# Performance work log

Hardware: AMD Instinct MI355X
Metric: run time of the kernel (lower is better)

The kernel has to match this reference:

```python
import jax, jax.numpy as jnp
import numpy as np

ALPHA_R = 0.1  # leak rate of rate variable r
ALPHA_S = 0.2  # leak rate of synaptic current I

B, T, IN, H, OUT = 32, 2048, 256, 1024, 128


def setup_inputs() -> dict:
    key = jax.random.key(0)
    k1, k2, k3, k4 = jax.random.split(key, 4)
    x = jax.random.normal(k1, (B, T, IN), dtype=jnp.float32)
    # Orthogonal-ish init approximated by scaled gaussians (spectral radius ~1)
    Win = jax.random.normal(k2, (H, IN), dtype=jnp.float32) / np.sqrt(IN)
    Wrec = jax.random.normal(k3, (H, H), dtype=jnp.float32) / np.sqrt(H)
    Wout = jax.random.uniform(k4, (OUT, H), dtype=jnp.float32)
    return {"x": x, "Win": Win, "Wrec": Wrec, "Wout": Wout}


def reference(x, Win, Wrec, Wout):
    # x: [B, T, IN]. State kept batch-major [B, H] (torch code uses [H, B]; same math transposed).
    b = x.shape[0]
    h = Wrec.shape[0]
    WinT, WrecT, WoutT = Win.T, Wrec.T, Wout.T

    def step(carry, xt):
        I, r = carry
        I = (1.0 - ALPHA_S) * I + ALPHA_S * (r @ WrecT + xt @ WinT)
        # r_t = (1-a_r) r + a_r tanh(I_t)
        r = (1.0 - ALPHA_R) * r + ALPHA_R * jnp.tanh(I)
        return (I, r), r @ WoutT  # out_t: [B, OUT]

    init = (jnp.zeros((b, h), x.dtype), jnp.zeros((b, h), x.dtype))
    _, ys = jax.lax.scan(step, init, jnp.swapaxes(x, 0, 1))  # ys: [T, B, OUT]
    return jnp.swapaxes(ys, 0, 1)  # [B, T, OUT]
```

## Files before the change

kernel.cpp:

```cpp
#include <hip/hip_runtime.h>
#include <math.h>


#define T_STEPS 2048
#define B_SZ 32
#define IN_SZ 256
#define H_SZ 1024
#define OUT_SZ 128
#define WGS 256
#define NWG 256
#define PB_WORDS (B_SZ * (H_SZ / 2))
#define WS_WORDS (2 * PB_WORDS)

typedef unsigned int u32;
typedef u32 u32x4 __attribute__((ext_vector_type(4)));
typedef float f32x4 __attribute__((ext_vector_type(4)));
typedef short s16x8 __attribute__((ext_vector_type(8)));

__global__ void nrnn_init_ws(u32* __restrict__ ws) {
  const int i = blockIdx.x * blockDim.x + threadIdx.x;
  if (i < WS_WORDS) ws[i] = 0x00000001u;
}

__device__ __forceinline__ u32 bf16r(float x) {
  const u32 b = __float_as_uint(x);
  return (b + 0x7FFFu + ((b >> 16) & 1u)) >> 16;
}
__device__ __forceinline__ void st_sys_u32(u32* p, u32 v) {
  __hip_atomic_store(p, v, __ATOMIC_RELAXED, __HIP_MEMORY_SCOPE_SYSTEM);
}
__device__ __forceinline__ float tanh_fast(float x) {
  const float cx = fminf(fmaxf(x, -15.f), 15.f);
  const float e = __expf(2.f * cx);
  return (e - 1.f) * __builtin_amdgcn_rcpf(e + 1.f);
}

__global__ void __launch_bounds__(WGS, 1)
nrnn_main(const float* __restrict__ x, const float* __restrict__ Win,
          const float* __restrict__ Wrec, const float* __restrict__ Wout,
          float* __restrict__ out, float* __restrict__ ws) {
  const int tid = (int)threadIdx.x;
  const int hg  = tid >> 5;
  const int s   = tid & 31;
  const int wv  = tid >> 6;
  const int ln  = tid & 63;
  const int bg  = (int)blockIdx.x & 7;
  const int jb  = (int)blockIdx.x >> 3;

  u32* pbuf = (u32*)ws;
  const int b0 = bg * 4;

  __shared__ __align__(16) char r_lds[4 * 2048];
  __shared__ float wacc_lds[2][32][4];
  __shared__ float4 padlds[4800];

  if (__float_as_uint(x[0]) == 0x7F800001u) padlds[tid].x = 1.f;

  s16x8 wfrag[32];
  {
    const int g = (ln >> 4) & 3;
    const float* wp;
    if (wv < 2)       wp = Wrec + (size_t)(jb * 32 + wv * 16 + (ln & 15)) * H_SZ;
    else if (wv == 2) wp = Wout + (size_t)(jb * 4 + (ln & 3)) * H_SZ;
    else              wp = Wrec;
    #pragma unroll
    for (int st = 0; st < 32; ++st) {
      const int k0 = st * 32 + g * 8;
      const float4 c0 = *(const float4*)(wp + k0);
      const float4 c1 = *(const float4*)(wp + k0 + 4);
      s16x8 w;
      w[0] = (short)bf16r(c0.x); w[1] = (short)bf16r(c0.y);
      w[2] = (short)bf16r(c0.z); w[3] = (short)bf16r(c0.w);
      w[4] = (short)bf16r(c1.x); w[5] = (short)bf16r(c1.y);
      w[6] = (short)bf16r(c1.z); w[7] = (short)bf16r(c1.w);
      wfrag[st] = w;
    }
  }

  float4 wi4[4][2];
  #pragma unroll
  for (int hh = 0; hh < 4; ++hh) {
    const float* ip = Win + (size_t)(jb * 32 + hg * 4 + hh) * IN_SZ + s * 4;
    wi4[hh][0] = *(const float4*)(ip);
    wi4[hh][1] = *(const float4*)(ip + 128);
  }

  float Ist[4] = {0.f, 0.f, 0.f, 0.f};
  float rloc[4] = {0.f, 0.f, 0.f, 0.f};

  {
    float wacc[4][4];
    #pragma unroll
    for (int b = 0; b < 4; ++b)
      #pragma unroll
      for (int hh = 0; hh < 4; ++hh) wacc[b][hh] = 0.f;
    #pragma unroll
    for (int b = 0; b < 4; ++b) {
      const float* xp = x + ((size_t)(b0 + b) * T_STEPS) * IN_SZ + s * 4;
      const float4 x0 = *(const float4*)(xp);
      const float4 x1 = *(const float4*)(xp + 128);
      #pragma unroll
      for (int hh = 0; hh < 4; ++hh) {
        float4 w4 = wi4[hh][0];
        wacc[b][hh] = fmaf(w4.x, x0.x, wacc[b][hh]);
        wacc[b][hh] = fmaf(w4.y, x0.y, wacc[b][hh]);
        wacc[b][hh] = fmaf(w4.z, x0.z, wacc[b][hh]);
        wacc[b][hh] = fmaf(w4.w, x0.w, wacc[b][hh]);
        w4 = wi4[hh][1];
        wacc[b][hh] = fmaf(w4.x, x1.x, wacc[b][hh]);
        wacc[b][hh] = fmaf(w4.y, x1.y, wacc[b][hh]);
        wacc[b][hh] = fmaf(w4.z, x1.z, wacc[b][hh]);
        wacc[b][hh] = fmaf(w4.w, x1.w, wacc[b][hh]);
      }
    }
    #pragma unroll
    for (int m = 1; m <= 16; m <<= 1)
      #pragma unroll
      for (int b = 0; b < 4; ++b)
        #pragma unroll
        for (int hh = 0; hh < 4; ++hh)
          wacc[b][hh] += __shfl_xor(wacc[b][hh], m, 64);
    if (s < 16) wacc_lds[0][hg * 4 + (s & 3)][s >> 2] = wacc[s >> 2][s & 3];
  }

  auto poll_stage = [&](int tcur) {
    const u32 etag = (((u32)(tcur - 1)) >> 1) & 1u;
    const u32* gp = pbuf + (size_t)((tcur + 1) & 1) * PB_WORDS + (size_t)bg * 2048u;
    const u32* p0 = gp + 4 * tid;
    const u32* p1 = gp + 1024 + 4 * tid;
    u32x4 a0, a1;
    bool ok;
    do {
      asm volatile(
          "global_load_dwordx4 %0, %2, off sc0 sc1\n\t"
          "global_load_dwordx4 %1, %3, off sc0 sc1\n\t"
          "s_waitcnt vmcnt(0)"
          : "=&v"(a0), "=&v"(a1) : "v"(p0), "v"(p1) : "memory");
      u32 bad = 0;
      #pragma unroll
      for (int i = 0; i < 4; ++i) { bad |= a0[i] ^ etag; bad |= a1[i] ^ etag; }
      ok = ((bad & 1u) == 0u);
    } while (__any(!ok));
    const int bi0 = tid >> 7, bi1 = 2 + (tid >> 7);
    *(u32x4*)(r_lds + ((16 * tid) ^ ((bi0 & 3) << 4) ^ ((bi0 & 1) << 6))) = a0;
    *(u32x4*)(r_lds + ((4096 + 16 * tid) ^ ((bi1 & 3) << 4) ^ ((bi1 & 1) << 6))) = a1;
  };

  for (int t = 0; t < T_STEPS; ++t) {
    const int tt = (t + 1 < T_STEPS) ? (t + 1) : (T_STEPS - 1);
    float4 xv[4][2];
    #pragma unroll
    for (int b = 0; b < 4; ++b) {
      const float* xp = x + ((size_t)(b0 + b) * T_STEPS + (size_t)tt) * IN_SZ + s * 4;
      xv[b][0] = *(const float4*)(xp);
      xv[b][1] = *(const float4*)(xp + 128);
    }

    poll_stage(t);
    __syncthreads();

    f32x4 acc = {0.f, 0.f, 0.f, 0.f};
    if (wv <= 2) {
      const int beff = ln & 3;
      const int g16 = ((ln >> 4) & 3) * 16;
      const int bswz = ((beff & 3) << 4) | ((beff & 1) << 6);
      const char* rb = r_lds + beff * 2048;
      #pragma unroll
      for (int st = 0; st < 32; ++st) {
        const s16x8 bf = *(const s16x8*)(rb + ((st * 64 + g16) ^ bswz));
        acc = __builtin_amdgcn_mfma_f32_16x16x32_bf16(wfrag[st], bf, acc, 0, 0, 0);
      }
    }

    if (wv < 2 && (ln & 12) == 0) {
      const int b = ln & 3;
      const int g = ln >> 4;
      const int rbase = wv * 16 + g * 4;
      const u32 ptag = (((u32)t) >> 1) & 1u;
      u32 pk0, pk1;
      {
        float In0 = fmaf(0.2f, acc[0] + wacc_lds[t & 1][rbase + 0][b], 0.8f * Ist[0]);
        float In1 = fmaf(0.2f, acc[1] + wacc_lds[t & 1][rbase + 1][b], 0.8f * Ist[1]);
        float In2 = fmaf(0.2f, acc[2] + wacc_lds[t & 1][rbase + 2][b], 0.8f * Ist[2]);
        float In3 = fmaf(0.2f, acc[3] + wacc_lds[t & 1][rbase + 3][b], 0.8f * Ist[3]);
        Ist[0] = In0; Ist[1] = In1; Ist[2] = In2; Ist[3] = In3;
        rloc[0] = fmaf(0.1f, tanh_fast(In0), 0.9f * rloc[0]);
        rloc[1] = fmaf(0.1f, tanh_fast(In1), 0.9f * rloc[1]);
        rloc[2] = fmaf(0.1f, tanh_fast(In2), 0.9f * rloc[2]);
        rloc[3] = fmaf(0.1f, tanh_fast(In3), 0.9f * rloc[3]);
        pk0 = ((bf16r(rloc[1]) << 16) | (bf16r(rloc[0]) & 0xFFFFu));
        pk0 = (pk0 & ~1u) | ptag;
        pk1 = ((bf16r(rloc[3]) << 16) | (bf16r(rloc[2]) & 0xFFFFu));
        pk1 = (pk1 & ~1u) | ptag;
      }
      u32* pw = pbuf + (size_t)(t & 1) * PB_WORDS
                + (size_t)(b0 + b) * 512 + jb * 16 + wv * 8 + g * 2;
      st_sys_u32(pw, pk0);
      st_sys_u32(pw + 1, pk1);
    }

    if (wv == 2 && ln < 4 && t > 0) {
      #pragma unroll
      for (int reg = 0; reg < 4; ++reg)
        out[((size_t)(b0 + ln) * T_STEPS + (size_t)(t - 1)) * OUT_SZ + jb * 4 + reg] = acc[reg];
    }

    {
      float wacc[4][4];
      #pragma unroll
      for (int b = 0; b < 4; ++b)
        #pragma unroll
        for (int hh = 0; hh < 4; ++hh) wacc[b][hh] = 0.f;
      #pragma unroll
      for (int b = 0; b < 4; ++b) {
        const float4 x0 = xv[b][0];
        const float4 x1 = xv[b][1];
        #pragma unroll
        for (int hh = 0; hh < 4; ++hh) {
          float4 w4 = wi4[hh][0];
          wacc[b][hh] = fmaf(w4.x, x0.x, wacc[b][hh]);
          wacc[b][hh] = fmaf(w4.y, x0.y, wacc[b][hh]);
          wacc[b][hh] = fmaf(w4.z, x0.z, wacc[b][hh]);
          wacc[b][hh] = fmaf(w4.w, x0.w, wacc[b][hh]);
          w4 = wi4[hh][1];
          wacc[b][hh] = fmaf(w4.x, x1.x, wacc[b][hh]);
          wacc[b][hh] = fmaf(w4.y, x1.y, wacc[b][hh]);
          wacc[b][hh] = fmaf(w4.z, x1.z, wacc[b][hh]);
          wacc[b][hh] = fmaf(w4.w, x1.w, wacc[b][hh]);
        }
      }
      #pragma unroll
      for (int m = 1; m <= 16; m <<= 1)
        #pragma unroll
        for (int b = 0; b < 4; ++b)
          #pragma unroll
          for (int hh = 0; hh < 4; ++hh)
            wacc[b][hh] += __shfl_xor(wacc[b][hh], m, 64);
      if (s < 16)
        wacc_lds[(t + 1) & 1][hg * 4 + (s & 3)][s >> 2] = wacc[s >> 2][s & 3];
    }

    __syncthreads();
  }

  poll_stage(T_STEPS);
  __syncthreads();
  {
    f32x4 acc = {0.f, 0.f, 0.f, 0.f};
    if (wv == 2) {
      const int beff = ln & 3;
      const int g16 = ((ln >> 4) & 3) * 16;
      const int bswz = ((beff & 3) << 4) | ((beff & 1) << 6);
      const char* rb = r_lds + beff * 2048;
      #pragma unroll
      for (int st = 0; st < 32; ++st) {
        const s16x8 bf = *(const s16x8*)(rb + ((st * 64 + g16) ^ bswz));
        acc = __builtin_amdgcn_mfma_f32_16x16x32_bf16(wfrag[st], bf, acc, 0, 0, 0);
      }
      if (ln < 4) {
        #pragma unroll
        for (int reg = 0; reg < 4; ++reg)
          out[((size_t)(b0 + ln) * T_STEPS + (size_t)(T_STEPS - 1)) * OUT_SZ + jb * 4 + reg] = acc[reg];
      }
    }
  }
}

extern "C" void kernel_launch(void* const* d_in, const int* in_sizes, int n_in,
                              void* d_out, int out_size, void* d_ws, size_t ws_size,
                              hipStream_t stream) {
  const float* xp    = (const float*)d_in[0];
  const float* winp  = (const float*)d_in[1];
  const float* wrecp = (const float*)d_in[2];
  const float* woutp = (const float*)d_in[3];
  float* outp = (float*)d_out;
  float* wsp  = (float*)d_ws;

  nrnn_init_ws<<<(WS_WORDS + 255) / 256, 256, 0, stream>>>((u32*)d_ws);

  nrnn_main<<<dim3(NWG), dim3(WGS), 0, stream>>>(xp, winp, wrecp, woutp, outp, wsp);
}
```

Measured before the change: 6.093 ms.

## Move input projection to bf16 MFMA and prefetch next-step state poll

The per-step Win·x projection moves from scalar FMAs with shuffle reductions into bf16 MFMA using preconverted Win fragments, and the wacc LDS staging is dropped. The first poll load for the next step's recurrent state is issued at the end of each iteration so its latency overlaps the barrier. The recurrent MFMA chain is split into two accumulators, and the state and output stores are widened to vector stores. The LDS padding used to force one block per CU is removed. Rounding x and Win to bf16 adds precision error compared with the fp32 input projection.

```diff
diff --git a/kernel.cpp b/kernel.cpp
--- a/kernel.cpp
+++ b/kernel.cpp
@@ -3,16 +3,16 @@
 
 
 #define T_STEPS 2048
-#define B_SZ 32
 #define IN_SZ 256
 #define H_SZ 1024
 #define OUT_SZ 128
 #define WGS 256
 #define NWG 256
-#define PB_WORDS (B_SZ * (H_SZ / 2))
+#define PB_WORDS 16384
 #define WS_WORDS (2 * PB_WORDS)
 
 typedef unsigned int u32;
+typedef u32 u32x2 __attribute__((ext_vector_type(2)));
 typedef u32 u32x4 __attribute__((ext_vector_type(4)));
 typedef float f32x4 __attribute__((ext_vector_type(4)));
 typedef short s16x8 __attribute__((ext_vector_type(8)));
@@ -22,15 +22,12 @@
   if (i < WS_WORDS) ws[i] = 0x00000001u;
 }
 
-__device__ __forceinline__ u32 bf16r(float x) {
-  const u32 b = __float_as_uint(x);
+__device__ __forceinline__ u32 bf16r(float v) {
+  const u32 b = __float_as_uint(v);
   return (b + 0x7FFFu + ((b >> 16) & 1u)) >> 16;
 }
-__device__ __forceinline__ void st_sys_u32(u32* p, u32 v) {
-  __hip_atomic_store(p, v, __ATOMIC_RELAXED, __HIP_MEMORY_SCOPE_SYSTEM);
-}
-__device__ __forceinline__ float tanh_fast(float x) {
-  const float cx = fminf(fmaxf(x, -15.f), 15.f);
+__device__ __forceinline__ float tanh_fast(float v) {
+  const float cx = fminf(fmaxf(v, -15.f), 15.f);
   const float e = __expf(2.f * cx);
   return (e - 1.f) * __builtin_amdgcn_rcpf(e + 1.f);
 }
@@ -40,21 +37,14 @@
           const float* __restrict__ Wrec, const float* __restrict__ Wout,
           float* __restrict__ out, float* __restrict__ ws) {
   const int tid = (int)threadIdx.x;
-  const int hg  = tid >> 5;
-  const int s   = tid & 31;
   const int wv  = tid >> 6;
   const int ln  = tid & 63;
   const int bg  = (int)blockIdx.x & 7;
   const int jb  = (int)blockIdx.x >> 3;
+  const int b0  = bg * 4;
 
   u32* pbuf = (u32*)ws;
-  const int b0 = bg * 4;
-
-  __shared__ __align__(16) char r_lds[4 * 2048];
-  __shared__ float wacc_lds[2][32][4];
-  __shared__ float4 padlds[4800];
-
-  if (__float_as_uint(x[0]) == 0x7F800001u) padlds[tid].x = 1.f;
+  __shared__ __align__(16) char r_lds[8192];
 
   s16x8 wfrag[32];
   {
@@ -77,87 +67,96 @@
     }
   }
 
-  float4 wi4[4][2];
-  #pragma unroll
-  for (int hh = 0; hh < 4; ++hh) {
-    const float* ip = Win + (size_t)(jb * 32 + hg * 4 + hh) * IN_SZ + s * 4;
-    wi4[hh][0] = *(const float4*)(ip);
-    wi4[hh][1] = *(const float4*)(ip + 128);
-  }
+  s16x8 wifrag[8];
+  if (wv < 2) {
+    const float* wp = Win + (size_t)(jb * 32 + wv * 16 + (ln & 15)) * IN_SZ
+                      + ((ln >> 4) & 3) * 8;
+    #pragma unroll
+    for (int ch = 0; ch < 8; ++ch) {
+      const float4 c0 = *(const float4*)(wp + ch * 32);
+      const float4 c1 = *(const float4*)(wp + ch * 32 + 4);
+      s16x8 w;
+      w[0] = (short)bf16r(c0.x); w[1] = (short)bf16r(c0.y);
+      w[2] = (short)bf16r(c0.z); w[3] = (short)bf16r(c0.w);
+      w[4] = (short)bf16r(c1.x); w[5] = (short)bf16r(c1.y);
+      w[6] = (short)bf16r(c1.z); w[7] = (short)bf16r(c1.w);
+      wifrag[ch] = w;
+    }
+  } else {
+    const s16x8 z = {0, 0, 0, 0, 0, 0, 0, 0};
+    #pragma unroll
+    for (int ch = 0; ch < 8; ++ch) wifrag[ch] = z;
+  }
+
+  auto ldx_issue = [&](int tt, float4 (&xv)[16]) {
+    if (wv < 2) {
+      const float* xb = x + ((size_t)(b0 + (ln & 3)) * T_STEPS + (size_t)tt) * IN_SZ
+                        + ((ln >> 4) & 3) * 8;
+      #pragma unroll
+      for (int ch = 0; ch < 8; ++ch) {
+        xv[2 * ch]     = *(const float4*)(xb + ch * 32);
+        xv[2 * ch + 1] = *(const float4*)(xb + ch * 32 + 4);
+      }
+    }
+  };
+  auto cvt = [&](const float4 (&xv)[16], u32x4 (&xf)[8]) {
+    if (wv < 2) {
+      #pragma unroll
+      for (int ch = 0; ch < 8; ++ch) {
+        u32x4 u;
+        u[0] = __builtin_amdgcn_perm(__float_as_uint(xv[2 * ch].y),
+                                     __float_as_uint(xv[2 * ch].x), 0x07060302u);
+        u[1] = __builtin_amdgcn_perm(__float_as_uint(xv[2 * ch].w),
+                                     __float_as_uint(xv[2 * ch].z), 0x07060302u);
+        u[2] = __builtin_amdgcn_perm(__float_as_uint(xv[2 * ch + 1].y),
+                                     __float_as_uint(xv[2 * ch + 1].x), 0x07060302u);
+        u[3] = __builtin_amdgcn_perm(__float_as_uint(xv[2 * ch + 1].w),
+                                     __float_as_uint(xv[2 * ch + 1].z), 0x07060302u);
+        xf[ch] = u;
+      }
+    }
+  };
 
   float Ist[4] = {0.f, 0.f, 0.f, 0.f};
   float rloc[4] = {0.f, 0.f, 0.f, 0.f};
 
-  {
-    float wacc[4][4];
-    #pragma unroll
-    for (int b = 0; b < 4; ++b)
-      #pragma unroll
-      for (int hh = 0; hh < 4; ++hh) wacc[b][hh] = 0.f;
-    #pragma unroll
-    for (int b = 0; b < 4; ++b) {
-      const float* xp = x + ((size_t)(b0 + b) * T_STEPS) * IN_SZ + s * 4;
-      const float4 x0 = *(const float4*)(xp);
-      const float4 x1 = *(const float4*)(xp + 128);
-      #pragma unroll
-      for (int hh = 0; hh < 4; ++hh) {
-        float4 w4 = wi4[hh][0];
-        wacc[b][hh] = fmaf(w4.x, x0.x, wacc[b][hh]);
-        wacc[b][hh] = fmaf(w4.y, x0.y, wacc[b][hh]);
-        wacc[b][hh] = fmaf(w4.z, x0.z, wacc[b][hh]);
-        wacc[b][hh] = fmaf(w4.w, x0.w, wacc[b][hh]);
-        w4 = wi4[hh][1];
-        wacc[b][hh] = fmaf(w4.x, x1.x, wacc[b][hh]);
-        wacc[b][hh] = fmaf(w4.y, x1.y, wacc[b][hh]);
-        wacc[b][hh] = fmaf(w4.z, x1.z, wacc[b][hh]);
-        wacc[b][hh] = fmaf(w4.w, x1.w, wacc[b][hh]);
-      }
-    }
-    #pragma unroll
-    for (int m = 1; m <= 16; m <<= 1)
-      #pragma unroll
-      for (int b = 0; b < 4; ++b)
-        #pragma unroll
-        for (int hh = 0; hh < 4; ++hh)
-          wacc[b][hh] += __shfl_xor(wacc[b][hh], m, 64);
-    if (s < 16) wacc_lds[0][hg * 4 + (s & 3)][s >> 2] = wacc[s >> 2][s & 3];
-  }
-
-  auto poll_stage = [&](int tcur) {
-    const u32 etag = (((u32)(tcur - 1)) >> 1) & 1u;
-    const u32* gp = pbuf + (size_t)((tcur + 1) & 1) * PB_WORDS + (size_t)bg * 2048u;
-    const u32* p0 = gp + 4 * tid;
-    const u32* p1 = gp + 1024 + 4 * tid;
-    u32x4 a0, a1;
-    bool ok;
-    do {
-      asm volatile(
-          "global_load_dwordx4 %0, %2, off sc0 sc1\n\t"
-          "global_load_dwordx4 %1, %3, off sc0 sc1\n\t"
-          "s_waitcnt vmcnt(0)"
-          : "=&v"(a0), "=&v"(a1) : "v"(p0), "v"(p1) : "memory");
+  u32x4 xf[8];
+  {
+    float4 xv0[16];
+    ldx_issue(0, xv0);
+    cvt(xv0, xf);
+  }
+  u32x4 swa, swb;
+  {
+    const u32* sp0 = pbuf + (size_t)PB_WORDS + (size_t)bg * 2048 + 4 * tid;
+    asm volatile("global_load_dwordx4 %0, %2, off sc0 sc1\n\t"
+                 "global_load_dwordx4 %1, %3, off sc0 sc1"
+                 : "=v"(swa), "=v"(swb) : "v"(sp0), "v"(sp0 + 1024) : "memory");
+  }
+
+  for (int t = 0; t < T_STEPS; ++t) {
+    const u32 etag = (((u32)(t - 1)) >> 1) & 1u;
+    const u32* sp0 = pbuf + (size_t)((t + 1) & 1) * PB_WORDS + (size_t)bg * 2048 + 4 * tid;
+    asm volatile("s_waitcnt vmcnt(0)" : "+v"(swa), "+v"(swb) :: "memory");
+    for (;;) {
       u32 bad = 0;
       #pragma unroll
-      for (int i = 0; i < 4; ++i) { bad |= a0[i] ^ etag; bad |= a1[i] ^ etag; }
-      ok = ((bad & 1u) == 0u);
-    } while (__any(!ok));
-    const int bi0 = tid >> 7, bi1 = 2 + (tid >> 7);
-    *(u32x4*)(r_lds + ((16 * tid) ^ ((bi0 & 3) << 4) ^ ((bi0 & 1) << 6))) = a0;
-    *(u32x4*)(r_lds + ((4096 + 16 * tid) ^ ((bi1 & 3) << 4) ^ ((bi1 & 1) << 6))) = a1;
-  };
-
-  for (int t = 0; t < T_STEPS; ++t) {
-    const int tt = (t + 1 < T_STEPS) ? (t + 1) : (T_STEPS - 1);
-    float4 xv[4][2];
-    #pragma unroll
-    for (int b = 0; b < 4; ++b) {
-      const float* xp = x + ((size_t)(b0 + b) * T_STEPS + (size_t)tt) * IN_SZ + s * 4;
-      xv[b][0] = *(const float4*)(xp);
-      xv[b][1] = *(const float4*)(xp + 128);
-    }
-
-    poll_stage(t);
+      for (int i = 0; i < 4; ++i) { bad |= swa[i] ^ etag; bad |= swb[i] ^ etag; }
+      if (!__any(bad & 1u)) break;
+      asm volatile("global_load_dwordx4 %0, %2, off sc0 sc1\n\t"
+                   "global_load_dwordx4 %1, %3, off sc0 sc1\n\t"
+                   "s_waitcnt vmcnt(0)"
+                   : "=&v"(swa), "=&v"(swb) : "v"(sp0), "v"(sp0 + 1024) : "memory");
+    }
+    {
+      const int bi0 = tid >> 7, bi1 = 2 + bi0;
+      *(u32x4*)(r_lds + ((16 * tid) ^ ((bi0 & 3) << 4) ^ ((bi0 & 1) << 6))) = swa;
+      *(u32x4*)(r_lds + ((4096 + 16 * tid) ^ ((bi1 & 3) << 4) ^ ((bi1 & 1) << 6))) = swb;
+    }
     __syncthreads();
+
+    float4 xv[16];
+    ldx_issue((t + 1 < T_STEPS) ? t + 1 : t, xv);
 
     f32x4 acc = {0.f, 0.f, 0.f, 0.f};
     if (wv <= 2) {
@@ -165,103 +164,97 @@
       const int g16 = ((ln >> 4) & 3) * 16;
       const int bswz = ((beff & 3) << 4) | ((beff & 1) << 6);
       const char* rb = r_lds + beff * 2048;
-      #pragma unroll
-      for (int st = 0; st < 32; ++st) {
-        const s16x8 bf = *(const s16x8*)(rb + ((st * 64 + g16) ^ bswz));
-        acc = __builtin_amdgcn_mfma_f32_16x16x32_bf16(wfrag[st], bf, acc, 0, 0, 0);
+      f32x4 a0 = {0.f, 0.f, 0.f, 0.f}, a1 = {0.f, 0.f, 0.f, 0.f};
+      #pragma unroll
+      for (int st = 0; st < 32; st += 2) {
+        const s16x8 bfa = *(const s16x8*)(rb + ((st * 64 + g16) ^ bswz));
+        const s16x8 bfb = *(const s16x8*)(rb + (((st + 1) * 64 + g16) ^ bswz));
+        a0 = __builtin_amdgcn_mfma_f32_16x16x32_bf16(wfrag[st], bfa, a0, 0, 0, 0);
+        a1 = __builtin_amdgcn_mfma_f32_16x16x32_bf16(wfrag[st + 1], bfb, a1, 0, 0, 0);
       }
+      acc = a0 + a1;
+    }
+
+    f32x4 wm = {0.f, 0.f, 0.f, 0.f};
+    if (wv < 2) {
+      #pragma unroll
+      for (int ch = 0; ch < 8; ++ch)
+        wm = __builtin_amdgcn_mfma_f32_16x16x32_bf16(wifrag[ch],
+                                                     *(const s16x8*)&xf[ch], wm, 0, 0, 0);
     }
 
     if (wv < 2 && (ln & 12) == 0) {
-      const int b = ln & 3;
-      const int g = ln >> 4;
-      const int rbase = wv * 16 + g * 4;
+      const int b = ln & 3, g4 = ln >> 4;
       const u32 ptag = (((u32)t) >> 1) & 1u;
-      u32 pk0, pk1;
-      {
-        float In0 = fmaf(0.2f, acc[0] + wacc_lds[t & 1][rbase + 0][b], 0.8f * Ist[0]);
-        float In1 = fmaf(0.2f, acc[1] + wacc_lds[t & 1][rbase + 1][b], 0.8f * Ist[1]);
-        float In2 = fmaf(0.2f, acc[2] + wacc_lds[t & 1][rbase + 2][b], 0.8f * Ist[2]);
-        float In3 = fmaf(0.2f, acc[3] + wacc_lds[t & 1][rbase + 3][b], 0.8f * Ist[3]);
-        Ist[0] = In0; Ist[1] = In1; Ist[2] = In2; Ist[3] = In3;
-        rloc[0] = fmaf(0.1f, tanh_fast(In0), 0.9f * rloc[0]);
-        rloc[1] = fmaf(0.1f, tanh_fast(In1), 0.9f * rloc[1]);
-        rloc[2] = fmaf(0.1f, tanh_fast(In2), 0.9f * rloc[2]);
-        rloc[3] = fmaf(0.1f, tanh_fast(In3), 0.9f * rloc[3]);
-        pk0 = ((bf16r(rloc[1]) << 16) | (bf16r(rloc[0]) & 0xFFFFu));
-        pk0 = (pk0 & ~1u) | ptag;
-        pk1 = ((bf16r(rloc[3]) << 16) | (bf16r(rloc[2]) & 0xFFFFu));
-        pk1 = (pk1 & ~1u) | ptag;
-      }
-      u32* pw = pbuf + (size_t)(t & 1) * PB_WORDS
-                + (size_t)(b0 + b) * 512 + jb * 16 + wv * 8 + g * 2;
-      st_sys_u32(pw, pk0);
-      st_sys_u32(pw + 1, pk1);
+      const float I0 = fmaf(0.2f, acc[0] + wm[0], 0.8f * Ist[0]);
+      const float I1 = fmaf(0.2f, acc[1] + wm[1], 0.8f * Ist[1]);
+      const float I2 = fmaf(0.2f, acc[2] + wm[2], 0.8f * Ist[2]);
+      const float I3 = fmaf(0.2f, acc[3] + wm[3], 0.8f * Ist[3]);
+      Ist[0] = I0; Ist[1] = I1; Ist[2] = I2; Ist[3] = I3;
+      rloc[0] = fmaf(0.1f, tanh_fast(I0), 0.9f * rloc[0]);
+      rloc[1] = fmaf(0.1f, tanh_fast(I1), 0.9f * rloc[1]);
+      rloc[2] = fmaf(0.1f, tanh_fast(I2), 0.9f * rloc[2]);
+      rloc[3] = fmaf(0.1f, tanh_fast(I3), 0.9f * rloc[3]);
+      u32x2 pk;
+      pk[0] = (((bf16r(rloc[1]) << 16) | (bf16r(rloc[0]) & 0xFFFFu)) & ~1u) | ptag;
+      pk[1] = (((bf16r(rloc[3]) << 16) | (bf16r(rloc[2]) & 0xFFFFu)) & ~1u) | ptag;
+      u32* pw = pbuf + (size_t)(t & 1) * PB_WORDS + (size_t)(b0 + b) * 512
+                + jb * 16 + wv * 8 + g4 * 2;
+      asm volatile("global_store_dwordx2 %0, %1, off sc0 sc1"
+                   :: "v"(pw), "v"(pk) : "memory");
     }
 
     if (wv == 2 && ln < 4 && t > 0) {
-      #pragma unroll
-      for (int reg = 0; reg < 4; ++reg)
-        out[((size_t)(b0 + ln) * T_STEPS + (size_t)(t - 1)) * OUT_SZ + jb * 4 + reg] = acc[reg];
-    }
+      float4 o; o.x = acc[0]; o.y = acc[1]; o.z = acc[2]; o.w = acc[3];
+      *(float4*)(out + ((size_t)(b0 + ln) * T_STEPS + (size_t)(t - 1)) * OUT_SZ
+                 + jb * 4) = o;
+    }
+
+    cvt(xv, xf);
 
     {
-      float wacc[4][4];
-      #pragma unroll
-      for (int b = 0; b < 4; ++b)
-        #pragma unroll
-        for (int hh = 0; hh < 4; ++hh) wacc[b][hh] = 0.f;
-      #pragma unroll
-      for (int b = 0; b < 4; ++b) {
-        const float4 x0 = xv[b][0];
-        const float4 x1 = xv[b][1];
-        #pragma unroll
-        for (int hh = 0; hh < 4; ++hh) {
-          float4 w4 = wi4[hh][0];
-          wacc[b][hh] = fmaf(w4.x, x0.x, wacc[b][hh]);
-          wacc[b][hh] = fmaf(w4.y, x0.y, wacc[b][hh]);
-          wacc[b][hh] = fmaf(w4.z, x0.z, wacc[b][hh]);
-          wacc[b][hh] = fmaf(w4.w, x0.w, wacc[b][hh]);
-          w4 = wi4[hh][1];
-          wacc[b][hh] = fmaf(w4.x, x1.x, wacc[b][hh]);
-          wacc[b][hh] = fmaf(w4.y, x1.y, wacc[b][hh]);
-          wacc[b][hh] = fmaf(w4.z, x1.z, wacc[b][hh]);
-          wacc[b][hh] = fmaf(w4.w, x1.w, wacc[b][hh]);
-        }
-      }
-      #pragma unroll
-      for (int m = 1; m <= 16; m <<= 1)
-        #pragma unroll
-        for (int b = 0; b < 4; ++b)
-          #pragma unroll
-          for (int hh = 0; hh < 4; ++hh)
-            wacc[b][hh] += __shfl_xor(wacc[b][hh], m, 64);
-      if (s < 16)
-        wacc_lds[(t + 1) & 1][hg * 4 + (s & 3)][s >> 2] = wacc[s >> 2][s & 3];
-    }
-
+      const u32* np0 = pbuf + (size_t)(t & 1) * PB_WORDS + (size_t)bg * 2048 + 4 * tid;
+      asm volatile("global_load_dwordx4 %0, %2, off sc0 sc1\n\t"
+                   "global_load_dwordx4 %1, %3, off sc0 sc1"
+                   : "=v"(swa), "=v"(swb) : "v"(np0), "v"(np0 + 1024) : "memory");
+    }
     __syncthreads();
   }
 
-  poll_stage(T_STEPS);
+  {
+    const u32 etag = (((u32)(T_STEPS - 1)) >> 1) & 1u;
+    const u32* sp0 = pbuf + (size_t)PB_WORDS + (size_t)bg * 2048 + 4 * tid;
+    asm volatile("s_waitcnt vmcnt(0)" : "+v"(swa), "+v"(swb) :: "memory");
+    for (;;) {
+      u32 bad = 0;
+      #pragma unroll
+      for (int i = 0; i < 4; ++i) { bad |= swa[i] ^ etag; bad |= swb[i] ^ etag; }
+      if (!__any(bad & 1u)) break;
+      asm volatile("global_load_dwordx4 %0, %2, off sc0 sc1\n\t"
+                   "global_load_dwordx4 %1, %3, off sc0 sc1\n\t"
+                   "s_waitcnt vmcnt(0)"
+                   : "=&v"(swa), "=&v"(swb) : "v"(sp0), "v"(sp0 + 1024) : "memory");
+    }
+    const int bi0 = tid >> 7, bi1 = 2 + bi0;
+    *(u32x4*)(r_lds + ((16 * tid) ^ ((bi0 & 3) << 4) ^ ((bi0 & 1) << 6))) = swa;
+    *(u32x4*)(r_lds + ((4096 + 16 * tid) ^ ((bi1 & 3) << 4) ^ ((bi1 & 1) << 6))) = swb;
+  }
   __syncthreads();
-  {
+  if (wv == 2) {
+    const int beff = ln & 3;
+    const int g16 = ((ln >> 4) & 3) * 16;
+    const int bswz = ((beff & 3) << 4) | ((beff & 1) << 6);
+    const char* rb = r_lds + beff * 2048;
     f32x4 acc = {0.f, 0.f, 0.f, 0.f};
-    if (wv == 2) {
-      const int beff = ln & 3;
-      const int g16 = ((ln >> 4) & 3) * 16;
-      const int bswz = ((beff & 3) << 4) | ((beff & 1) << 6);
-      const char* rb = r_lds + beff * 2048;
-      #pragma unroll
-      for (int st = 0; st < 32; ++st) {
-        const s16x8 bf = *(const s16x8*)(rb + ((st * 64 + g16) ^ bswz));
-        acc = __builtin_amdgcn_mfma_f32_16x16x32_bf16(wfrag[st], bf, acc, 0, 0, 0);
-      }
-      if (ln < 4) {
-        #pragma unroll
-        for (int reg = 0; reg < 4; ++reg)
-          out[((size_t)(b0 + ln) * T_STEPS + (size_t)(T_STEPS - 1)) * OUT_SZ + jb * 4 + reg] = acc[reg];
-      }
+    #pragma unroll
+    for (int st = 0; st < 32; ++st) {
+      const s16x8 bf = *(const s16x8*)(rb + ((st * 64 + g16) ^ bswz));
+      acc = __builtin_amdgcn_mfma_f32_16x16x32_bf16(wfrag[st], bf, acc, 0, 0, 0);
+    }
+    if (ln < 4) {
+      float4 o; o.x = acc[0]; o.y = acc[1]; o.z = acc[2]; o.w = acc[3];
+      *(float4*)(out + ((size_t)(b0 + ln) * T_STEPS + (size_t)(T_STEPS - 1)) * OUT_SZ
+                 + jb * 4) = o;
     }
   }
 }
```

After: 5.505 ms. 9.6% less time.
